# Optimization experiments

Measured on AMD Instinct MI355X. Metric: run time of the kernel, lower is better.

Reference implementation:

```python
import jax, jax.numpy as jnp
import numpy as np

HIDDEN = 128
N_HEADS = 8
SEQ = 4096


def setup_inputs() -> dict:
    key = jax.random.key(0)
    ks = jax.random.split(key, 7)
    H, NH = HIDDEN, N_HEADS
    s = 1.0 / np.sqrt(H)
    return {
        "x": jax.random.normal(ks[0], (SEQ, H), dtype=jnp.float32),
        "W1": jax.random.uniform(ks[1], (H, H * NH), jnp.float32, -s, s),
        "b1": jax.random.uniform(ks[2], (H * NH,), jnp.float32, -s, s),
        "W2": jax.random.uniform(ks[3], (H, H * NH), jnp.float32, -s, s),
        "b2": jax.random.uniform(ks[4], (H * NH,), jnp.float32, -s, s),
        "Wc": jax.random.uniform(ks[5], (H * NH, H), jnp.float32, -1.0 / np.sqrt(H * NH), 1.0 / np.sqrt(H * NH)),
        "bc": jax.random.uniform(ks[6], (H,), jnp.float32, -1.0 / np.sqrt(H * NH), 1.0 / np.sqrt(H * NH)),
    }


def reference(x, W1, b1, W2, b2, Wc, bc):
    S, H = x.shape
    NH = W1.shape[1] // H
    # project then split into heads: [S, NH*H] -> [NH, S, H]
    q1 = (x @ W1 + b1).reshape(S, NH, H).transpose(1, 0, 2)
    q2 = (x @ W2 + b2).reshape(S, NH, H).transpose(1, 0, 2)
    # unscaled attention scores per head: [NH, S, S]
    att = jax.nn.softmax(jnp.einsum('hse,hte->hst', q1, q2), axis=-1)
    # weighted sum of q2 (values == q2 in this module): [NH, S, H]
    ctx = jnp.einsum('hst,hte->hse', att, q2)
    # concat heads back along feature dim: [S, NH*H]
    ctx = ctx.transpose(1, 0, 2).reshape(S, NH * H)
    return ctx @ Wc + bc + x
```

## Files before the change

kernel.cpp:

```cpp
#include <hip/hip_runtime.h>

#define H 128
#define NHEADS 8
#define SQ 4096
#define HD 1024

typedef float f32x4 __attribute__((ext_vector_type(4)));
typedef __bf16 bf16x8 __attribute__((ext_vector_type(8)));
typedef unsigned short u16x4 __attribute__((ext_vector_type(4)));
typedef unsigned short u16x8 __attribute__((ext_vector_type(8)));

static __device__ __forceinline__ unsigned short f2bf(float f) {
  unsigned int u = __builtin_bit_cast(unsigned int, f);
  u += 0x7fffu + ((u >> 16) & 1u);
  return (unsigned short)(u >> 16);
}
static __device__ __forceinline__ float b2f(unsigned short s) {
  unsigned int u = (unsigned int)s << 16;
  return __builtin_bit_cast(float, u);
}
static __device__ __forceinline__ bf16x8 ld_bf8(const unsigned short* p) {
  return __builtin_bit_cast(bf16x8, *(const u16x8*)p);
}

__global__ __launch_bounds__(256) void prep_kernel(
    const float* __restrict__ W1, const float* __restrict__ W2,
    const float* __restrict__ Wc,
    unsigned short* __restrict__ W1T, unsigned short* __restrict__ W2T,
    unsigned short* __restrict__ WcT)
{
  __shared__ unsigned short tile[64 * 66];
  const int b = blockIdx.x, tid = threadIdx.x;
  if (b < 32) {
    const int k0 = (b & 1) * 64, n0 = (b >> 1) * 64;
    for (int i = 0; i < 16; ++i) {
      int idx = tid + i * 256;
      int r = idx >> 6, cc = idx & 63;
      tile[cc * 66 + r] = f2bf(W1[(size_t)(k0 + r) * HD + n0 + cc]);
    }
    __syncthreads();
    for (int i = 0; i < 16; ++i) {
      int idx = tid + i * 256;
      int r = idx >> 6, cc = idx & 63;
      W1T[(size_t)(n0 + r) * H + k0 + cc] = tile[r * 66 + cc];
    }
    __syncthreads();
    for (int i = 0; i < 16; ++i) {
      int idx = tid + i * 256;
      int r = idx >> 6, cc = idx & 63;
      tile[cc * 66 + r] = f2bf(W2[(size_t)(k0 + r) * HD + n0 + cc]);
    }
    __syncthreads();
    for (int i = 0; i < 16; ++i) {
      int idx = tid + i * 256;
      int r = idx >> 6, cc = idx & 63;
      W2T[(size_t)(n0 + r) * H + k0 + cc] = tile[r * 66 + cc];
    }
  } else {
    const int bb = b - 32;
    const int n0 = (bb & 1) * 64, k0 = (bb >> 1) * 64;
    for (int i = 0; i < 16; ++i) {
      int idx = tid + i * 256;
      int r = idx >> 6, cc = idx & 63;
      tile[cc * 66 + r] = f2bf(Wc[(size_t)(k0 + r) * H + n0 + cc]);
    }
    __syncthreads();
    for (int i = 0; i < 16; ++i) {
      int idx = tid + i * 256;
      int r = idx >> 6, cc = idx & 63;
      WcT[(size_t)(n0 + r) * HD + k0 + cc] = tile[r * 66 + cc];
    }
  }
}

__global__ __launch_bounds__(256) void proj_kernel(
    const float* __restrict__ x,
    const float* __restrict__ b1, const float* __restrict__ b2,
    const unsigned short* __restrict__ W1T, const unsigned short* __restrict__ W2T,
    unsigned short* __restrict__ q1bf, unsigned short* __restrict__ q2K,
    unsigned short* __restrict__ q2VT)
{
  __shared__ unsigned short At[64 * 136];
  __shared__ unsigned short Bt[128 * 136];
  const int tid = threadIdx.x;
  const int st = blockIdx.x & 63, h = blockIdx.x >> 6;
  const int s0 = st * 64;
  const int lane = tid & 63, w = tid >> 6;
  const int c = lane & 15, q4 = lane >> 4;

  for (int i = 0; i < 4; ++i) {
    int ch = tid + i * 256;
    int row = ch >> 4, col8 = (ch & 15) * 8;
    const float* gp = x + (s0 + row) * H + col8;
    f32x4 a = *(const f32x4*)gp;
    f32x4 b = *(const f32x4*)(gp + 4);
    u16x8 v;
    v[0]=f2bf(a[0]); v[1]=f2bf(a[1]); v[2]=f2bf(a[2]); v[3]=f2bf(a[3]);
    v[4]=f2bf(b[0]); v[5]=f2bf(b[1]); v[6]=f2bf(b[2]); v[7]=f2bf(b[3]);
    *(u16x8*)&At[row * 136 + col8] = v;
  }
  for (int i = 0; i < 8; ++i) {
    int ch = tid + i * 256;
    int row = ch >> 4, col8 = (ch & 15) * 8;
    *(u16x8*)&Bt[row * 136 + col8] = *(const u16x8*)&W1T[(h * H + row) * H + col8];
  }
  __syncthreads();

  bf16x8 af[4];
  for (int kc = 0; kc < 4; ++kc)
    af[kc] = ld_bf8(&At[(w * 16 + c) * 136 + kc * 32 + q4 * 8]);
  __syncthreads();

  for (int nt = 0; nt < 8; ++nt) {
    f32x4 acc = {0.f, 0.f, 0.f, 0.f};
    for (int kc = 0; kc < 4; ++kc) {
      bf16x8 bf = ld_bf8(&Bt[(nt * 16 + c) * 136 + kc * 32 + q4 * 8]);
      acc = __builtin_amdgcn_mfma_f32_16x16x32_bf16(af[kc], bf, acc, 0, 0, 0);
    }
    float bb = b1[h * H + nt * 16 + c];
    for (int r = 0; r < 4; ++r)
      At[(w * 16 + q4 * 4 + r) * 136 + nt * 16 + c] = f2bf(acc[r] + bb);
  }
  __syncthreads();

  for (int i = 0; i < 4; ++i) {
    int ch = tid + i * 256;
    int row = ch >> 4, col8 = (ch & 15) * 8;
    *(u16x8*)&q1bf[(size_t)(h * SQ + s0 + row) * H + col8] =
        *(const u16x8*)&At[row * 136 + col8];
  }
  for (int i = 0; i < 8; ++i) {
    int ch = tid + i * 256;
    int row = ch >> 4, col8 = (ch & 15) * 8;
    *(u16x8*)&Bt[row * 136 + col8] = *(const u16x8*)&W2T[(h * H + row) * H + col8];
  }
  __syncthreads();

  f32x4 q2a[8];
  for (int nt = 0; nt < 8; ++nt) {
    f32x4 acc = {0.f, 0.f, 0.f, 0.f};
    for (int kc = 0; kc < 4; ++kc) {
      bf16x8 bf = ld_bf8(&Bt[(nt * 16 + c) * 136 + kc * 32 + q4 * 8]);
      acc = __builtin_amdgcn_mfma_f32_16x16x32_bf16(af[kc], bf, acc, 0, 0, 0);
    }
    q2a[nt] = acc;
  }
  __syncthreads();

  for (int nt = 0; nt < 8; ++nt) {
    float bb = b2[h * H + nt * 16 + c];
    unsigned short vs[4];
    for (int r = 0; r < 4; ++r) {
      unsigned short u = f2bf(q2a[nt][r] + bb);
      At[(w * 16 + q4 * 4 + r) * 136 + nt * 16 + c] = u;
      vs[r] = u;
    }
    u16x4 v4 = {vs[0], vs[1], vs[2], vs[3]};
    *(u16x4*)&Bt[(nt * 16 + c) * 72 + w * 16 + q4 * 4] = v4;
  }
  __syncthreads();

  for (int i = 0; i < 4; ++i) {
    int ch = tid + i * 256;
    int row = ch >> 4, col8 = (ch & 15) * 8;
    *(u16x8*)&q2K[(size_t)(h * SQ + s0 + row) * H + col8] =
        *(const u16x8*)&At[row * 136 + col8];
  }
  for (int i = 0; i < 4; ++i) {
    int ch = tid + i * 256;
    int row = ch >> 3, col8 = (ch & 7) * 8;
    *(u16x8*)&q2VT[(size_t)(h * H + row) * SQ + s0 + col8] =
        *(const u16x8*)&Bt[row * 72 + col8];
  }
}

__global__ __launch_bounds__(256, 2) void flash_kernel(
    const unsigned short* __restrict__ q1bf,
    const unsigned short* __restrict__ q2K,
    const unsigned short* __restrict__ q2VT,
    unsigned short* __restrict__ ctxp,
    float* __restrict__ lbuf)
{
  __shared__ unsigned short Kt[64 * 152];
  __shared__ unsigned short VT[128 * 88];
  __shared__ unsigned short Pb[4][2][16 * 72];
  const int tid = threadIdx.x;
  const int bid = blockIdx.x;
  const int kb = bid >> 8;
  const int h = (bid >> 5) & 7, qb = bid & 31;
  const int s0 = qb * 128;
  const int kbase = kb * 2048;
  const int lane = tid & 63, w = tid >> 6;
  const int c = lane & 15, q4 = lane >> 4;

  bf16x8 qf[2][4];
  for (int blk = 0; blk < 2; ++blk)
    for (int kc = 0; kc < 4; ++kc)
      qf[blk][kc] = ld_bf8(
          &q1bf[(h * SQ + s0 + w * 32 + blk * 16 + c) * H + kc * 32 + q4 * 8]);

  f32x4 acc[2][8];
  for (int blk = 0; blk < 2; ++blk)
    for (int nt = 0; nt < 8; ++nt) acc[blk][nt] = (f32x4){0.f, 0.f, 0.f, 0.f};
  float lsum[2] = {0.f, 0.f};

  u16x8 kreg[4], vreg[4];
  for (int i = 0; i < 4; ++i) {
    int ch = tid + i * 256;
    kreg[i] = *(const u16x8*)&q2K[(h * SQ + kbase + (ch >> 4)) * H + (ch & 15) * 8];
    vreg[i] = *(const u16x8*)&q2VT[(h * H + (ch >> 3)) * SQ + kbase + (ch & 7) * 8];
  }

  for (int kt = 0; kt < 32; ++kt) {
    if (kt) __syncthreads();
    for (int i = 0; i < 4; ++i) {
      int ch = tid + i * 256;
      *(u16x8*)&Kt[(ch >> 4) * 152 + (ch & 15) * 8] = kreg[i];
      *(u16x8*)&VT[(ch >> 3) * 88 + (ch & 7) * 8] = vreg[i];
    }
    __syncthreads();

    if (kt < 31) {
      const int k0 = kbase + (kt + 1) * 64;
      for (int i = 0; i < 4; ++i) {
        int ch = tid + i * 256;
        kreg[i] = *(const u16x8*)&q2K[(h * SQ + k0 + (ch >> 4)) * H + (ch & 15) * 8];
        vreg[i] = *(const u16x8*)&q2VT[(h * H + (ch >> 3)) * SQ + k0 + (ch & 7) * 8];
      }
    }

    f32x4 sc[2][4];
    for (int mt = 0; mt < 4; ++mt) {
      bf16x8 kf[4];
      for (int kc = 0; kc < 4; ++kc)
        kf[kc] = ld_bf8(&Kt[(mt * 16 + c) * 152 + kc * 32 + q4 * 8]);
      for (int blk = 0; blk < 2; ++blk) {
        f32x4 s = {0.f, 0.f, 0.f, 0.f};
        for (int kc = 0; kc < 4; ++kc)
          s = __builtin_amdgcn_mfma_f32_16x16x32_bf16(kf[kc], qf[blk][kc], s, 0, 0, 0);
        sc[blk][mt] = s;
      }
    }

    for (int blk = 0; blk < 2; ++blk) {
      float ts = 0.f;
      for (int mt = 0; mt < 4; ++mt) {
        f32x4 p;
        for (int r = 0; r < 4; ++r) { p[r] = __expf(sc[blk][mt][r]); ts += p[r]; }
        sc[blk][mt] = p;
      }
      lsum[blk] += ts;
      for (int mt = 0; mt < 4; ++mt) {
        u16x4 pv = {f2bf(sc[blk][mt][0]), f2bf(sc[blk][mt][1]),
                    f2bf(sc[blk][mt][2]), f2bf(sc[blk][mt][3])};
        *(u16x4*)&Pb[w][blk][c * 72 + mt * 16 + q4 * 4] = pv;
      }
    }

    for (int kc2 = 0; kc2 < 2; ++kc2) {
      bf16x8 pf0 = ld_bf8(&Pb[w][0][c * 72 + kc2 * 32 + q4 * 8]);
      bf16x8 pf1 = ld_bf8(&Pb[w][1][c * 72 + kc2 * 32 + q4 * 8]);
      for (int nt = 0; nt < 8; ++nt) {
        bf16x8 vf = ld_bf8(&VT[(nt * 16 + c) * 88 + kc2 * 32 + q4 * 8]);
        acc[0][nt] = __builtin_amdgcn_mfma_f32_16x16x32_bf16(pf0, vf, acc[0][nt], 0, 0, 0);
        acc[1][nt] = __builtin_amdgcn_mfma_f32_16x16x32_bf16(pf1, vf, acc[1][nt], 0, 0, 0);
      }
    }
  }

  unsigned short* ctxk = ctxp + (size_t)kb * SQ * HD;
  for (int blk = 0; blk < 2; ++blk) {
    float l = lsum[blk];
    l += __shfl_xor(l, 16);
    l += __shfl_xor(l, 32);
    float rl = 1.f / l;
    if (q4 == 0)
      lbuf[(size_t)kb * NHEADS * SQ + h * SQ + s0 + w * 32 + blk * 16 + c] = l;
    float r0 = __shfl(rl, q4 * 4 + 0);
    float r1 = __shfl(rl, q4 * 4 + 1);
    float r2 = __shfl(rl, q4 * 4 + 2);
    float r3 = __shfl(rl, q4 * 4 + 3);
    for (int nt = 0; nt < 8; ++nt) {
      int col = h * H + nt * 16 + c;
      int srow = s0 + w * 32 + blk * 16 + q4 * 4;
      ctxk[(size_t)(srow + 0) * HD + col] = f2bf(acc[blk][nt][0] * r0);
      ctxk[(size_t)(srow + 1) * HD + col] = f2bf(acc[blk][nt][1] * r1);
      ctxk[(size_t)(srow + 2) * HD + col] = f2bf(acc[blk][nt][2] * r2);
      ctxk[(size_t)(srow + 3) * HD + col] = f2bf(acc[blk][nt][3] * r3);
    }
  }
}

__global__ __launch_bounds__(256) void out_kernel(
    const unsigned short* __restrict__ ctxp,
    const float* __restrict__ lbuf,
    const unsigned short* __restrict__ WcT,
    const float* __restrict__ bc,
    const float* __restrict__ x,
    float* __restrict__ out)
{
  __shared__ unsigned short At[64 * 136];
  __shared__ unsigned short Bt[128 * 136];
  const int tid = threadIdx.x;
  const int s0 = blockIdx.x * 64;
  const int lane = tid & 63, w = tid >> 6;
  const int c = lane & 15, q4 = lane >> 4;

  f32x4 acc[8];
  for (int nt = 0; nt < 8; ++nt) acc[nt] = (f32x4){0.f, 0.f, 0.f, 0.f};

  for (int kt = 0; kt < 8; ++kt) {
    __syncthreads();
    for (int i = 0; i < 4; ++i) {
      int ch = tid + i * 256;
      int row = ch >> 4, col8 = (ch & 15) * 8;
      const unsigned short* p0 = &ctxp[(size_t)(s0 + row) * HD + kt * 128 + col8];
      u16x8 a0 = *(const u16x8*)p0;
      u16x8 a1 = *(const u16x8*)(p0 + (size_t)SQ * HD);
      float la = lbuf[(size_t)kt * SQ + s0 + row];
      float lb = lbuf[(size_t)NHEADS * SQ + (size_t)kt * SQ + s0 + row];
      float ri = 1.f / (la + lb);
      float wa = la * ri, wb = lb * ri;
      u16x8 av;
      for (int e = 0; e < 8; ++e)
        av[e] = f2bf(wa * b2f(a0[e]) + wb * b2f(a1[e]));
      *(u16x8*)&At[row * 136 + col8] = av;
    }
    for (int i = 0; i < 8; ++i) {
      int ch = tid + i * 256;
      int row = ch >> 4, col8 = (ch & 15) * 8;
      *(u16x8*)&Bt[row * 136 + col8] =
          *(const u16x8*)&WcT[row * HD + kt * 128 + col8];
    }
    __syncthreads();
    bf16x8 af[4];
    for (int kc = 0; kc < 4; ++kc)
      af[kc] = ld_bf8(&At[(w * 16 + c) * 136 + kc * 32 + q4 * 8]);
    for (int nt = 0; nt < 8; ++nt) {
      f32x4 a = acc[nt];
      for (int kc = 0; kc < 4; ++kc) {
        bf16x8 bf = ld_bf8(&Bt[(nt * 16 + c) * 136 + kc * 32 + q4 * 8]);
        a = __builtin_amdgcn_mfma_f32_16x16x32_bf16(af[kc], bf, a, 0, 0, 0);
      }
      acc[nt] = a;
    }
  }
  for (int nt = 0; nt < 8; ++nt) {
    float bb = bc[nt * 16 + c];
    for (int r = 0; r < 4; ++r) {
      int srow = s0 + w * 16 + q4 * 4 + r;
      int col = nt * 16 + c;
      out[srow * H + col] = acc[nt][r] + bb + x[srow * H + col];
    }
  }
}

extern "C" void kernel_launch(void* const* d_in, const int* in_sizes, int n_in,
                              void* d_out, int out_size, void* d_ws, size_t ws_size,
                              hipStream_t stream) {
  const float* x  = (const float*)d_in[0];
  const float* W1 = (const float*)d_in[1];
  const float* b1 = (const float*)d_in[2];
  const float* W2 = (const float*)d_in[3];
  const float* b2 = (const float*)d_in[4];
  const float* Wc = (const float*)d_in[5];
  const float* bc = (const float*)d_in[6];
  float* out = (float*)d_out;

  char* ws = (char*)d_ws;
  unsigned short* q1bf = (unsigned short*)ws; ws += (size_t)NHEADS * SQ * H * 2;
  unsigned short* q2K  = (unsigned short*)ws; ws += (size_t)NHEADS * SQ * H * 2;
  unsigned short* q2VT = (unsigned short*)ws; ws += (size_t)NHEADS * SQ * H * 2;
  unsigned short* ctxp = (unsigned short*)ws; ws += (size_t)2 * SQ * HD * 2;
  float*          lbuf = (float*)ws;          ws += (size_t)2 * NHEADS * SQ * 4;
  unsigned short* W1T  = (unsigned short*)ws; ws += (size_t)HD * H * 2;
  unsigned short* W2T  = (unsigned short*)ws; ws += (size_t)HD * H * 2;
  unsigned short* WcT  = (unsigned short*)ws; ws += (size_t)HD * H * 2;

  prep_kernel<<<64, 256, 0, stream>>>(W1, W2, Wc, W1T, W2T, WcT);
  proj_kernel<<<512, 256, 0, stream>>>(x, b1, b2, W1T, W2T, q1bf, q2K, q2VT);
  flash_kernel<<<512, 256, 0, stream>>>(q1bf, q2K, q2VT, ctxp, lbuf);
  out_kernel<<<64, 256, 0, stream>>>(ctxp, lbuf, WcT, bc, x, out);
}
```

Before: 207.8 us.

## Use 8 waves per flash block with one 16-row query tile each

Restructures the flash attention kernel from 4 waves each handling two 16-row query blocks to 8 waves each handling one block, with 512 threads per workgroup. This halves per-thread accumulator and Q-fragment registers, which should allow more waves per CU to hide memory and exp latency. In exchange, each K/V fragment loaded from shared memory is reused across only one query block instead of two, roughly doubling LDS reads per MFMA, and the block-wide barriers now synchronise twice as many waves.

```diff
diff --git a/kernel.cpp b/kernel.cpp
--- a/kernel.cpp
+++ b/kernel.cpp
@@ -174,7 +174,7 @@
   }
 }
 
-__global__ __launch_bounds__(256, 2) void flash_kernel(
+__global__ __launch_bounds__(512, 4) void flash_kernel(
     const unsigned short* __restrict__ q1bf,
     const unsigned short* __restrict__ q2K,
     const unsigned short* __restrict__ q2VT,
@@ -183,7 +183,7 @@
 {
   __shared__ unsigned short Kt[64 * 152];
   __shared__ unsigned short VT[128 * 88];
-  __shared__ unsigned short Pb[4][2][16 * 72];
+  __shared__ unsigned short Pb[8][16 * 72];
   const int tid = threadIdx.x;
   const int bid = blockIdx.x;
   const int kb = bid >> 8;
@@ -193,28 +193,26 @@
   const int lane = tid & 63, w = tid >> 6;
   const int c = lane & 15, q4 = lane >> 4;
 
-  bf16x8 qf[2][4];
-  for (int blk = 0; blk < 2; ++blk)
-    for (int kc = 0; kc < 4; ++kc)
-      qf[blk][kc] = ld_bf8(
-          &q1bf[(h * SQ + s0 + w * 32 + blk * 16 + c) * H + kc * 32 + q4 * 8]);
-
-  f32x4 acc[2][8];
-  for (int blk = 0; blk < 2; ++blk)
-    for (int nt = 0; nt < 8; ++nt) acc[blk][nt] = (f32x4){0.f, 0.f, 0.f, 0.f};
-  float lsum[2] = {0.f, 0.f};
-
-  u16x8 kreg[4], vreg[4];
-  for (int i = 0; i < 4; ++i) {
-    int ch = tid + i * 256;
+  bf16x8 qf[4];
+  for (int kc = 0; kc < 4; ++kc)
+    qf[kc] = ld_bf8(
+        &q1bf[(h * SQ + s0 + w * 16 + c) * H + kc * 32 + q4 * 8]);
+
+  f32x4 acc[8];
+  for (int nt = 0; nt < 8; ++nt) acc[nt] = (f32x4){0.f, 0.f, 0.f, 0.f};
+  float lsum = 0.f;
+
+  u16x8 kreg[2], vreg[2];
+  for (int i = 0; i < 2; ++i) {
+    int ch = tid + i * 512;
     kreg[i] = *(const u16x8*)&q2K[(h * SQ + kbase + (ch >> 4)) * H + (ch & 15) * 8];
     vreg[i] = *(const u16x8*)&q2VT[(h * H + (ch >> 3)) * SQ + kbase + (ch & 7) * 8];
   }
 
   for (int kt = 0; kt < 32; ++kt) {
     if (kt) __syncthreads();
-    for (int i = 0; i < 4; ++i) {
-      int ch = tid + i * 256;
+    for (int i = 0; i < 2; ++i) {
+      int ch = tid + i * 512;
       *(u16x8*)&Kt[(ch >> 4) * 152 + (ch & 15) * 8] = kreg[i];
       *(u16x8*)&VT[(ch >> 3) * 88 + (ch & 7) * 8] = vreg[i];
     }
@@ -222,71 +220,67 @@
 
     if (kt < 31) {
       const int k0 = kbase + (kt + 1) * 64;
-      for (int i = 0; i < 4; ++i) {
-        int ch = tid + i * 256;
+      for (int i = 0; i < 2; ++i) {
+        int ch = tid + i * 512;
         kreg[i] = *(const u16x8*)&q2K[(h * SQ + k0 + (ch >> 4)) * H + (ch & 15) * 8];
         vreg[i] = *(const u16x8*)&q2VT[(h * H + (ch >> 3)) * SQ + k0 + (ch & 7) * 8];
       }
     }
 
-    f32x4 sc[2][4];
+    f32x4 sc[4];
     for (int mt = 0; mt < 4; ++mt) {
       bf16x8 kf[4];
       for (int kc = 0; kc < 4; ++kc)
         kf[kc] = ld_bf8(&Kt[(mt * 16 + c) * 152 + kc * 32 + q4 * 8]);
-      for (int blk = 0; blk < 2; ++blk) {
-        f32x4 s = {0.f, 0.f, 0.f, 0.f};
-        for (int kc = 0; kc < 4; ++kc)
-          s = __builtin_amdgcn_mfma_f32_16x16x32_bf16(kf[kc], qf[blk][kc], s, 0, 0, 0);
-        sc[blk][mt] = s;
-      }
-    }
-
-    for (int blk = 0; blk < 2; ++blk) {
+      f32x4 s = {0.f, 0.f, 0.f, 0.f};
+      for (int kc = 0; kc < 4; ++kc)
+        s = __builtin_amdgcn_mfma_f32_16x16x32_bf16(kf[kc], qf[kc], s, 0, 0, 0);
+      sc[mt] = s;
+    }
+
+    {
       float ts = 0.f;
       for (int mt = 0; mt < 4; ++mt) {
         f32x4 p;
-        for (int r = 0; r < 4; ++r) { p[r] = __expf(sc[blk][mt][r]); ts += p[r]; }
-        sc[blk][mt] = p;
-      }
-      lsum[blk] += ts;
+        for (int r = 0; r < 4; ++r) { p[r] = __expf(sc[mt][r]); ts += p[r]; }
+        sc[mt] = p;
+      }
+      lsum += ts;
       for (int mt = 0; mt < 4; ++mt) {
-        u16x4 pv = {f2bf(sc[blk][mt][0]), f2bf(sc[blk][mt][1]),
-                    f2bf(sc[blk][mt][2]), f2bf(sc[blk][mt][3])};
-        *(u16x4*)&Pb[w][blk][c * 72 + mt * 16 + q4 * 4] = pv;
+        u16x4 pv = {f2bf(sc[mt][0]), f2bf(sc[mt][1]),
+                    f2bf(sc[mt][2]), f2bf(sc[mt][3])};
+        *(u16x4*)&Pb[w][c * 72 + mt * 16 + q4 * 4] = pv;
       }
     }
 
     for (int kc2 = 0; kc2 < 2; ++kc2) {
-      bf16x8 pf0 = ld_bf8(&Pb[w][0][c * 72 + kc2 * 32 + q4 * 8]);
-      bf16x8 pf1 = ld_bf8(&Pb[w][1][c * 72 + kc2 * 32 + q4 * 8]);
+      bf16x8 pf = ld_bf8(&Pb[w][c * 72 + kc2 * 32 + q4 * 8]);
       for (int nt = 0; nt < 8; ++nt) {
         bf16x8 vf = ld_bf8(&VT[(nt * 16 + c) * 88 + kc2 * 32 + q4 * 8]);
-        acc[0][nt] = __builtin_amdgcn_mfma_f32_16x16x32_bf16(pf0, vf, acc[0][nt], 0, 0, 0);
-        acc[1][nt] = __builtin_amdgcn_mfma_f32_16x16x32_bf16(pf1, vf, acc[1][nt], 0, 0, 0);
+        acc[nt] = __builtin_amdgcn_mfma_f32_16x16x32_bf16(pf, vf, acc[nt], 0, 0, 0);
       }
     }
   }
 
   unsigned short* ctxk = ctxp + (size_t)kb * SQ * HD;
-  for (int blk = 0; blk < 2; ++blk) {
-    float l = lsum[blk];
+  {
+    float l = lsum;
     l += __shfl_xor(l, 16);
     l += __shfl_xor(l, 32);
     float rl = 1.f / l;
     if (q4 == 0)
-      lbuf[(size_t)kb * NHEADS * SQ + h * SQ + s0 + w * 32 + blk * 16 + c] = l;
+      lbuf[(size_t)kb * NHEADS * SQ + h * SQ + s0 + w * 16 + c] = l;
     float r0 = __shfl(rl, q4 * 4 + 0);
     float r1 = __shfl(rl, q4 * 4 + 1);
     float r2 = __shfl(rl, q4 * 4 + 2);
     float r3 = __shfl(rl, q4 * 4 + 3);
     for (int nt = 0; nt < 8; ++nt) {
       int col = h * H + nt * 16 + c;
-      int srow = s0 + w * 32 + blk * 16 + q4 * 4;
-      ctxk[(size_t)(srow + 0) * HD + col] = f2bf(acc[blk][nt][0] * r0);
-      ctxk[(size_t)(srow + 1) * HD + col] = f2bf(acc[blk][nt][1] * r1);
-      ctxk[(size_t)(srow + 2) * HD + col] = f2bf(acc[blk][nt][2] * r2);
-      ctxk[(size_t)(srow + 3) * HD + col] = f2bf(acc[blk][nt][3] * r3);
+      int srow = s0 + w * 16 + q4 * 4;
+      ctxk[(size_t)(srow + 0) * HD + col] = f2bf(acc[nt][0] * r0);
+      ctxk[(size_t)(srow + 1) * HD + col] = f2bf(acc[nt][1] * r1);
+      ctxk[(size_t)(srow + 2) * HD + col] = f2bf(acc[nt][2] * r2);
+      ctxk[(size_t)(srow + 3) * HD + col] = f2bf(acc[nt][3] * r3);
     }
   }
 }
@@ -379,6 +373,6 @@
 
   prep_kernel<<<64, 256, 0, stream>>>(W1, W2, Wc, W1T, W2T, WcT);
   proj_kernel<<<512, 256, 0, stream>>>(x, b1, b2, W1T, W2T, q1bf, q2K, q2VT);
-  flash_kernel<<<512, 256, 0, stream>>>(q1bf, q2K, q2VT, ctxp, lbuf);
+  flash_kernel<<<512, 512, 0, stream>>>(q1bf, q2K, q2VT, ctxp, lbuf);
   out_kernel<<<64, 256, 0, stream>>>(ctxp, lbuf, WcT, bc, x, out);
 }
```

New measurement: 214.2 us. 3.1% more time.
